# Performance work log

Measured on AMD Instinct MI355X. Metric: run time of the kernel, lower is better.

Reference implementation:

```python
import jax, jax.numpy as jnp
import numpy as np

B, T, C, HS = 4, 512, 128, 64

def setup_inputs() -> dict:
    key = jax.random.key(0)
    ks = jax.random.split(key, 8)
    s1 = 1.0 / np.sqrt(2 * C)  # torch Linear default init scale ~ U(-1/sqrt(in),1/sqrt(in))
    s2 = 1.0 / np.sqrt(C)
    return {
        "x": jax.random.normal(ks[0], (B, T, C), jnp.float32),
        "pos_emb": jax.random.normal(ks[1], (T, C), jnp.float32),
        # att2 layer 1: Linear(2C -> C); stored as [2C, C] (in, out)
        "W1": jax.random.uniform(ks[2], (2 * C, C), jnp.float32, -s1, s1),
        "b1": jax.random.uniform(ks[3], (C,), jnp.float32, -s1, s1),
        # att2 layer 2: Linear(C -> 1)
        "W2": jax.random.uniform(ks[4], (C, 1), jnp.float32, -s2, s2),
        "b2": jax.random.uniform(ks[5], (1,), jnp.float32, -s2, s2),
        # value: Linear(C -> HS, bias=False)
        "Wv": jax.random.uniform(ks[6], (C, HS), jnp.float32, -s2, s2),
    }


def reference(x, pos_emb, W1, b1, W2, b2, Wv):
    b, t, c = x.shape
    x1 = pos_emb + x  # [b,t,c]
    # Pairwise feature: cat([x1[j], x1[i]], -1) at position [i, j].
    # First Linear on the concat splits into two [c,c] blocks -> avoids
    # materializing the [b,t,t,2c] concat while computing identical math.
    W1k, W1q = W1[:c], W1[c:]            # rows for k-part (x1[j]) and q-part (x1[i])
    Ak = jnp.einsum('bjc,cd->bjd', x1, W1k)  # [b,t,c] contribution from key index j
    Aq = jnp.einsum('bic,cd->bid', x1, W1q)  # [b,t,c] contribution from query index i
    hidden = jax.nn.relu(Aq[:, :, None, :] + Ak[:, None, :, :] + b1)  # [b,t,t,c]
    wei = (jnp.einsum('bijc,co->bijo', hidden, W2)[..., 0] + b2[0]) * (c ** -0.5)  # [b,t,t]
    # causal mask (tril)
    mask = jnp.tril(jnp.ones((t, t), dtype=bool))
    wei = jnp.where(mask, wei, -jnp.inf)
    wei = jax.nn.softmax(wei, axis=-1)
    v = jnp.einsum('btc,ch->bth', x, Wv)  # [b,t,hs]
    out = jnp.einsum('bij,bjh->bih', wei, v)
    return out
```

## Files before the change

kernel.cpp:

```cpp
#include <hip/hip_runtime.h>
#include <math.h>

#define B_ 4
#define T_ 512
#define C_ 128
#define HS_ 64

typedef float f4 __attribute__((ext_vector_type(4)));
typedef float f2 __attribute__((ext_vector_type(2)));

#define SCALE_ 0.08838834764831845f

static __device__ __forceinline__ f2 relu2(f2 v) {
    v.x = fmaxf(v.x, 0.f);
    v.y = fmaxf(v.y, 0.f);
    return v;
}

__global__ __launch_bounds__(640) void k_prep(
    const float* __restrict__ x, const float* __restrict__ pos,
    const float* __restrict__ W1, const float* __restrict__ b1,
    const float* __restrict__ Wv,
    float* __restrict__ Aq, float* __restrict__ AkT, float* __restrict__ V)
{
    __shared__ float x1s[8 * 132];
    __shared__ float xs[8 * 132];
    const int t = threadIdx.x;
    const int row0 = blockIdx.x * 8;

    if (t < 256) {
        int r = t >> 5, cq = t & 31;
        int gr = row0 + r;
        f4 xv = *(const f4*)(x + gr * 128 + cq * 4);
        f4 pv = *(const f4*)(pos + (gr & 511) * 128 + cq * 4);
        *(f4*)&xs[r * 132 + cq * 4] = xv;
        *(f4*)&x1s[r * 132 + cq * 4] = xv + pv;
    }
    __syncthreads();

    const int q = t >> 3;
    const int r = t & 7;

    const float* wbase;
    int wstr, col0;
    const float* xb;
    f4 binit = {0.f, 0.f, 0.f, 0.f};
    if (q < 32) {
        col0 = q * 4;
        wbase = W1 + 128 * 128 + col0;
        wstr = 128;
        xb = x1s;
        binit = *(const f4*)(b1 + col0);
    } else if (q < 64) {
        col0 = (q - 32) * 4;
        wbase = W1 + col0;
        wstr = 128;
        xb = x1s;
    } else {
        col0 = (q - 64) * 4;
        wbase = Wv + col0;
        wstr = 64;
        xb = xs;
    }

    f4 acc = binit;
    const float* xr = xb + r * 132;
#pragma unroll 8
    for (int c = 0; c < 128; ++c) {
        f4 w = *(const f4*)(wbase + c * wstr);
        acc += xr[c] * w;
    }

    const int gr = row0 + r;
    if (q < 32) {
        *(f4*)(Aq + (size_t)gr * 128 + col0) = acc;
    } else if (q < 64) {
        const int bb = gr >> 9, j = gr & 511;
        float* base = AkT + ((size_t)bb * 128 + col0) * 512 + j;
        base[0]    = acc.x;
        base[512]  = acc.y;
        base[1024] = acc.z;
        base[1536] = acc.w;
    } else {
        *(f4*)(V + (size_t)gr * 64 + col0) = acc;
    }
}

__global__ __launch_bounds__(256, 4) void k_fused(
    const float* __restrict__ Aq, const float* __restrict__ AkT,
    const float* __restrict__ Vv, const float* __restrict__ W2,
    float* __restrict__ out)
{
    __shared__ float pbuf[4][4][128];
    __shared__ float accs[4][4][64];
    __shared__ float mls[4][4][2];

    const int t = threadIdx.x;
    const int bx = blockIdx.x;
    const int b = bx & 3;
    const int g = 127 - (bx >> 2);
    const int r0 = g * 4;
    const int w = t >> 6, lane = t & 63;

    const int nj = r0 + 4;
    const int cj = ((nj + 7) >> 3) << 1;
    const int jstart = w * cj;
    const int jend = min(jstart + cj, nj);
    const int jA = jstart + lane * 2;

    float m0 = -1e30f, m1 = -1e30f, m2 = -1e30f, m3 = -1e30f;
    float l0 = 0.f, l1 = 0.f, l2 = 0.f, l3 = 0.f;
    float a0 = 0.f, a1 = 0.f, a2 = 0.f, a3 = 0.f;

    if (jstart < jend) {
        const float* aq0 = Aq + (size_t)(b * 512 + r0) * 128;
        const float* aq1 = aq0 + 128;
        const float* aq2 = aq1 + 128;
        const float* aq3 = aq2 + 128;
        const float* akt = AkT + (size_t)b * 65536 + jA;

        f2 s0a = {0,0}, s0b = {0,0}, s1a = {0,0}, s1b = {0,0};
        f2 s2a = {0,0}, s2b = {0,0}, s3a = {0,0}, s3b = {0,0};
#pragma unroll 4
        for (int c = 0; c < 128; c += 2) {
            const f2 k0 = *(const f2*)(akt + (size_t)c * 512);
            const f2 k1 = *(const f2*)(akt + (size_t)(c + 1) * 512);
            const float w0 = W2[c], w1 = W2[c + 1];
            s0a += relu2(k0 + aq0[c]) * w0;  s0b += relu2(k1 + aq0[c + 1]) * w1;
            s1a += relu2(k0 + aq1[c]) * w0;  s1b += relu2(k1 + aq1[c + 1]) * w1;
            s2a += relu2(k0 + aq2[c]) * w0;  s2b += relu2(k1 + aq2[c + 1]) * w1;
            s3a += relu2(k0 + aq3[c]) * w0;  s3b += relu2(k1 + aq3[c + 1]) * w1;
        }

#define FINROW(R, SA, SB, MD, LD)                                        \
        {                                                                \
            const int rr_ = r0 + (R);                                    \
            const int jlim_ = min(jend - 1, rr_);                        \
            f2 sv = (SA + SB) * SCALE_;                                  \
            float sx = (jA     <= jlim_) ? sv.x : -1e30f;                \
            float sy = (jA + 1 <= jlim_) ? sv.y : -1e30f;                \
            float mx = fmaxf(sx, sy);                                    \
            _Pragma("unroll")                                            \
            for (int off = 1; off < 64; off <<= 1)                       \
                mx = fmaxf(mx, __shfl_xor(mx, off));                     \
            const bool live_ = (jstart <= rr_);                          \
            const float px = live_ ? __expf(sx - mx) : 0.f;              \
            const float py = live_ ? __expf(sy - mx) : 0.f;              \
            f2 pp = {px, py};                                            \
            *(f2*)&pbuf[w][R][lane * 2] = pp;                            \
            float ls = px + py;                                          \
            _Pragma("unroll")                                            \
            for (int off = 1; off < 64; off <<= 1)                       \
                ls += __shfl_xor(ls, off);                               \
            MD = live_ ? mx : -1e30f;                                    \
            LD = ls;                                                     \
        }
        FINROW(0, s0a, s0b, m0, l0)
        FINROW(1, s1a, s1b, m1, l1)
        FINROW(2, s2a, s2b, m2, l2)
        FINROW(3, s3a, s3b, m3, l3)
#undef FINROW

        const float* vt = Vv + ((size_t)b * 512 + jstart) * 64 + lane;
        const int q4max = (jend - jstart + 3) >> 2;
        for (int q4 = 0; q4 < q4max; ++q4) {
            const f4 p0 = *(const f4*)&pbuf[w][0][q4 * 4];
            const f4 p1 = *(const f4*)&pbuf[w][1][q4 * 4];
            const f4 p2 = *(const f4*)&pbuf[w][2][q4 * 4];
            const f4 p3 = *(const f4*)&pbuf[w][3][q4 * 4];
            const float v0 = vt[(q4 * 4 + 0) * 64];
            const float v1 = vt[(q4 * 4 + 1) * 64];
            const float v2 = vt[(q4 * 4 + 2) * 64];
            const float v3 = vt[(q4 * 4 + 3) * 64];
            a0 += p0.x * v0 + p0.y * v1 + p0.z * v2 + p0.w * v3;
            a1 += p1.x * v0 + p1.y * v1 + p1.z * v2 + p1.w * v3;
            a2 += p2.x * v0 + p2.y * v1 + p2.z * v2 + p2.w * v3;
            a3 += p3.x * v0 + p3.y * v1 + p3.z * v2 + p3.w * v3;
        }
    }

    accs[w][0][lane] = a0;
    accs[w][1][lane] = a1;
    accs[w][2][lane] = a2;
    accs[w][3][lane] = a3;
    if (lane == 0) {
        mls[w][0][0] = m0; mls[w][0][1] = l0;
        mls[w][1][0] = m1; mls[w][1][1] = l1;
        mls[w][2][0] = m2; mls[w][2][1] = l2;
        mls[w][3][0] = m3; mls[w][3][1] = l3;
    }
    __syncthreads();

    const int rr = r0 + w;
    float ms = -1e30f;
#pragma unroll
    for (int ww = 0; ww < 4; ++ww) ms = fmaxf(ms, mls[ww][w][0]);
    float num = 0.f, den = 0.f;
#pragma unroll
    for (int ww = 0; ww < 4; ++ww) {
        const float e = __expf(mls[ww][w][0] - ms);
        den += mls[ww][w][1] * e;
        num += accs[ww][w][lane] * e;
    }
    out[(size_t)(b * 512 + rr) * 64 + lane] = num / den;
}

extern "C" void kernel_launch(void* const* d_in, const int* in_sizes, int n_in,
                              void* d_out, int out_size, void* d_ws, size_t ws_size,
                              hipStream_t stream)
{
    const float* x   = (const float*)d_in[0];
    const float* pos = (const float*)d_in[1];
    const float* W1  = (const float*)d_in[2];
    const float* b1  = (const float*)d_in[3];
    const float* W2  = (const float*)d_in[4];
    const float* b2  = (const float*)d_in[5];  (void)b2;
    const float* Wv  = (const float*)d_in[6];
    float* out = (float*)d_out;
    float* ws = (float*)d_ws;

    float* Aq  = ws;
    float* AkT = ws + 262144;
    float* V   = ws + 524288;

    k_prep<<<dim3(256), dim3(640), 0, stream>>>(x, pos, W1, b1, Wv, Aq, AkT, V);
    k_fused<<<dim3(512), dim3(256), 0, stream>>>(Aq, AkT, V, W2, out);
}
```

Measured before the change: 33.63 us.

## Stage Aq and W2 in LDS and double-buffer AkT loads in fused kernel

Each block now copies its four Aq rows and W2 into shared memory once and reads them as vectorised LDS loads, replacing the scalar global loads in the inner loop. The AkT loads are split into groups of 16 channels and prefetched one group ahead in a register double buffer, so global latency overlaps the relu/FMA work. The larger register footprint is allowed for by lowering the launch-bounds occupancy hint from 4 to 2 blocks, which may cut latency hiding elsewhere.

Result: no change. 33.81 us (+0.5%).

```diff
diff --git a/kernel.cpp b/kernel.cpp
--- a/kernel.cpp
+++ b/kernel.cpp
@@ -86,11 +86,13 @@
     }
 }
 
-__global__ __launch_bounds__(256, 4) void k_fused(
+__global__ __launch_bounds__(256, 2) void k_fused(
     const float* __restrict__ Aq, const float* __restrict__ AkT,
     const float* __restrict__ Vv, const float* __restrict__ W2,
     float* __restrict__ out)
 {
+    __shared__ float aqs[4][128];
+    __shared__ float w2s[128];
     __shared__ float pbuf[4][4][128];
     __shared__ float accs[4][4][64];
     __shared__ float mls[4][4][2];
@@ -102,6 +104,16 @@
     const int r0 = g * 4;
     const int w = t >> 6, lane = t & 63;
 
+    if (t < 128) {
+        const int r = t >> 5, cq = t & 31;
+        *(f4*)&aqs[r][cq * 4] =
+            *(const f4*)(Aq + (size_t)(b * 512 + r0 + r) * 128 + cq * 4);
+    } else if (t < 160) {
+        const int cq = t - 128;
+        *(f4*)&w2s[cq * 4] = *(const f4*)(W2 + cq * 4);
+    }
+    __syncthreads();
+
     const int nj = r0 + 4;
     const int cj = ((nj + 7) >> 3) << 1;
     const int jstart = w * cj;
@@ -113,23 +125,51 @@
     float a0 = 0.f, a1 = 0.f, a2 = 0.f, a3 = 0.f;
 
     if (jstart < jend) {
-        const float* aq0 = Aq + (size_t)(b * 512 + r0) * 128;
-        const float* aq1 = aq0 + 128;
-        const float* aq2 = aq1 + 128;
-        const float* aq3 = aq2 + 128;
         const float* akt = AkT + (size_t)b * 65536 + jA;
 
-        f2 s0a = {0,0}, s0b = {0,0}, s1a = {0,0}, s1b = {0,0};
-        f2 s2a = {0,0}, s2b = {0,0}, s3a = {0,0}, s3b = {0,0};
-#pragma unroll 4
-        for (int c = 0; c < 128; c += 2) {
-            const f2 k0 = *(const f2*)(akt + (size_t)c * 512);
-            const f2 k1 = *(const f2*)(akt + (size_t)(c + 1) * 512);
-            const float w0 = W2[c], w1 = W2[c + 1];
-            s0a += relu2(k0 + aq0[c]) * w0;  s0b += relu2(k1 + aq0[c + 1]) * w1;
-            s1a += relu2(k0 + aq1[c]) * w0;  s1b += relu2(k1 + aq1[c + 1]) * w1;
-            s2a += relu2(k0 + aq2[c]) * w0;  s2b += relu2(k1 + aq2[c + 1]) * w1;
-            s3a += relu2(k0 + aq3[c]) * w0;  s3b += relu2(k1 + aq3[c + 1]) * w1;
+        f2 kk[2][16];
+#pragma unroll
+        for (int i = 0; i < 16; ++i)
+            kk[0][i] = *(const f2*)(akt + i * 512);
+
+        f2 c0a = {0,0}, c0b = {0,0}, c1a = {0,0}, c1b = {0,0};
+        f2 c2a = {0,0}, c2b = {0,0}, c3a = {0,0}, c3b = {0,0};
+
+#pragma unroll
+        for (int grp = 0; grp < 8; ++grp) {
+            const int cur = grp & 1;
+            const int nxt = cur ^ 1;
+            if (grp < 7) {
+#pragma unroll
+                for (int i = 0; i < 16; ++i)
+                    kk[nxt][i] =
+                        *(const f2*)(akt + ((grp + 1) * 16 + i) * 512);
+            }
+#pragma unroll
+            for (int qi = 0; qi < 4; ++qi) {
+                const int c0 = grp * 16 + qi * 4;
+                const f4 q0 = *(const f4*)&aqs[0][c0];
+                const f4 q1 = *(const f4*)&aqs[1][c0];
+                const f4 q2 = *(const f4*)&aqs[2][c0];
+                const f4 q3 = *(const f4*)&aqs[3][c0];
+                const f4 wq = *(const f4*)&w2s[c0];
+#pragma unroll
+                for (int ch = 0; ch < 4; ++ch) {
+                    const f2 k = kk[cur][qi * 4 + ch];
+                    const float wv = wq[ch];
+                    if (ch & 1) {
+                        c0b += relu2(k + q0[ch]) * wv;
+                        c1b += relu2(k + q1[ch]) * wv;
+                        c2b += relu2(k + q2[ch]) * wv;
+                        c3b += relu2(k + q3[ch]) * wv;
+                    } else {
+                        c0a += relu2(k + q0[ch]) * wv;
+                        c1a += relu2(k + q1[ch]) * wv;
+                        c2a += relu2(k + q2[ch]) * wv;
+                        c3a += relu2(k + q3[ch]) * wv;
+                    }
+                }
+            }
         }
 
 #define FINROW(R, SA, SB, MD, LD)                                        \
@@ -155,10 +195,10 @@
             MD = live_ ? mx : -1e30f;                                    \
             LD = ls;                                                     \
         }
-        FINROW(0, s0a, s0b, m0, l0)
-        FINROW(1, s1a, s1b, m1, l1)
-        FINROW(2, s2a, s2b, m2, l2)
-        FINROW(3, s3a, s3b, m3, l3)
+        FINROW(0, c0a, c0b, m0, l0)
+        FINROW(1, c1a, c1b, m1, l1)
+        FINROW(2, c2a, c2b, m2, l2)
+        FINROW(3, c3a, c3b, m3, l3)
 #undef FINROW
 
         const float* vt = Vv + ((size_t)b * 512 + jstart) * 64 + lane;
```
